# Performance work log

Hardware: AMD Instinct MI355X
Metric: run time of the kernel (lower is better)

Reference implementation:

```python
import jax, jax.numpy as jnp
import numpy as np

N_ADDR = 400000
N_TX = 400000
E = 1500000
F_IN = 64
HID = 32
OUT = 2


def _sage(x_src, x_dst, ei, Wl, bl, Wr, n_dst):
    # SAGEConv: mean-aggregate source feats over incoming edges, then
    # out = lin_l(agg) + lin_r(x_dst). Nodes with no in-edges get agg=0.
    src, dst = ei[0], ei[1]
    msg = x_src[src]                                            # [E, F]
    s = jax.ops.segment_sum(msg, dst, num_segments=n_dst)       # [N_dst, F]
    cnt = jax.ops.segment_sum(jnp.ones((ei.shape[1], 1), x_src.dtype), dst,
                              num_segments=n_dst)               # [N_dst, 1]
    agg = s / jnp.maximum(cnt, 1.0)
    return agg @ Wl + bl + x_dst @ Wr


def setup_inputs() -> dict:
    key = jax.random.key(0)
    ks = jax.random.split(key, 24)
    d = {}
    d['x_addr'] = jax.random.normal(ks[0], (N_ADDR, F_IN), jnp.float32)
    d['x_tx'] = jax.random.normal(ks[1], (N_TX, F_IN), jnp.float32)
    d['ei_at'] = jax.random.randint(ks[2], (2, E), 0, N_ADDR)   # addr->tx (src idx < N_ADDR, dst idx < N_TX)
    d['ei_ta'] = jax.random.randint(ks[3], (2, E), 0, N_TX)     # tx->addr
    def w(k, i, o):
        return jax.random.normal(k, (i, o), jnp.float32) * (1.0 / np.sqrt(i))
    d['w1_tx_l'] = w(ks[4], F_IN, HID); d['b1_tx'] = jnp.zeros((HID,), jnp.float32)
    d['w1_tx_r'] = w(ks[5], F_IN, HID)
    d['w1_ad_l'] = w(ks[6], F_IN, HID); d['b1_ad'] = jnp.zeros((HID,), jnp.float32)
    d['w1_ad_r'] = w(ks[7], F_IN, HID)
    d['w2_tx_l'] = w(ks[8], HID, HID); d['b2_tx'] = jnp.zeros((HID,), jnp.float32)
    d['w2_tx_r'] = w(ks[9], HID, HID)
    d['w2_ad_l'] = w(ks[10], HID, HID); d['b2_ad'] = jnp.zeros((HID,), jnp.float32)
    d['w2_ad_r'] = w(ks[11], HID, HID)
    d['w3_tx_l'] = w(ks[12], HID, HID); d['b3_tx'] = jnp.zeros((HID,), jnp.float32)
    d['w3_tx_r'] = w(ks[13], HID, HID)
    d['w3_ad_l'] = w(ks[14], HID, HID); d['b3_ad'] = jnp.zeros((HID,), jnp.float32)
    d['w3_ad_r'] = w(ks[15], HID, HID)
    d['w_out'] = w(ks[16], HID, OUT); d['b_out'] = jnp.zeros((OUT,), jnp.float32)
    return d


def reference(x_addr, x_tx, ei_at, ei_ta,
              w1_tx_l, b1_tx, w1_tx_r, w1_ad_l, b1_ad, w1_ad_r,
              w2_tx_l, b2_tx, w2_tx_r, w2_ad_l, b2_ad, w2_ad_r,
              w3_tx_l, b3_tx, w3_tx_r, w3_ad_l, b3_ad, w3_ad_r,
              w_out, b_out):
    # Layer 1 (both node types updated simultaneously from previous x_dict)
    tx = jax.nn.relu(_sage(x_addr, x_tx, ei_at, w1_tx_l, b1_tx, w1_tx_r, N_TX))
    ad = jax.nn.relu(_sage(x_tx, x_addr, ei_ta, w1_ad_l, b1_ad, w1_ad_r, N_ADDR))
    # Layer 2
    tx2 = jax.nn.relu(_sage(ad, tx, ei_at, w2_tx_l, b2_tx, w2_tx_r, N_TX))
    ad2 = jax.nn.relu(_sage(tx, ad, ei_ta, w2_ad_l, b2_ad, w2_ad_r, N_ADDR))
    # Layer 3
    ad3 = jax.nn.relu(_sage(tx2, ad2, ei_ta, w3_ad_l, b3_ad, w3_ad_r, N_ADDR))
    # Final classifier on 'addr' nodes (dropout is identity at inference)
    return ad3 @ w_out + b_out
```

## Files before the change

### kernel.cpp

```cpp
#include <hip/hip_runtime.h>

#define NADDR 400000
#define NTX   400000
#define NEDGE 1500000
#define FIN   64
#define HID   32
#define NB    1563
#define LSTR  36
#define HSTR  36
#define NND   400000

static inline int cdiv_host(long a, int b) { return (int)((a + b - 1) / b); }

__device__ __forceinline__ unsigned short f2bf(float f) {
    unsigned b = __float_as_uint(f);
    b += 0x7FFFu + ((b >> 16) & 1u);
    return (unsigned short)(b >> 16);
}
__device__ __forceinline__ float bf2f(unsigned short s) {
    return __uint_as_float(((unsigned)s) << 16);
}


__global__ void k_hist(const int* __restrict__ at_dst, const int* __restrict__ ta_dst,
                       int* __restrict__ bcnt , int GH) {
    __shared__ int h[NB];
    bool wh = blockIdx.x >= GH;
    int blk = blockIdx.x - (wh ? GH : 0);
    const int* dst = wh ? ta_dst : at_dst;
    for (int i = threadIdx.x; i < NB; i += 256) h[i] = 0;
    __syncthreads();
    for (long e = (long)blk * 256 + threadIdx.x; e < NEDGE; e += (long)GH * 256)
        atomicAdd(&h[dst[e] >> 8], 1);
    __syncthreads();
    int* g = bcnt + (wh ? NB : 0);
    for (int i = threadIdx.x; i < NB; i += 256) {
        int v = h[i];
        if (v) atomicAdd(&g[i], v);
    }
}

__global__ void k_scan_nb(const int* __restrict__ bcnt, int* __restrict__ bbase,
                          int* __restrict__ gcur) {
    __shared__ int sm[256];
    __shared__ int carry;
    int w = blockIdx.x;
    int t = threadIdx.x;
    if (t == 0) carry = 0;
    __syncthreads();
    for (int base = 0; base < NB; base += 256) {
        int i = base + t;
        int v = (i < NB) ? bcnt[w * NB + i] : 0;
        sm[t] = v;
        __syncthreads();
        for (int off = 1; off < 256; off <<= 1) {
            int x = (t >= off) ? sm[t - off] : 0;
            __syncthreads();
            sm[t] += x;
            __syncthreads();
        }
        int excl = sm[t] - v + carry;
        if (i < NB) { bbase[w * (NB + 1) + i] = excl; gcur[w * NB + i] = excl; }
        int tot = sm[255];
        __syncthreads();
        if (t == 0) carry += tot;
        __syncthreads();
    }
    if (t == 0) bbase[w * (NB + 1) + NB] = NEDGE;
}

__global__ void k_dist(const int* __restrict__ ei_at, const int* __restrict__ ei_ta,
                       int* __restrict__ gcur, unsigned* __restrict__ eb_at,
                       unsigned* __restrict__ eb_ta, int GD) {
    __shared__ int h[NB];
    __shared__ int bs[NB];
    bool wh = blockIdx.x >= GD;
    int blk = blockIdx.x - (wh ? GD : 0);
    const int* ei = wh ? ei_ta : ei_at;
    unsigned* eb = wh ? eb_ta : eb_at;
    for (int i = threadIdx.x; i < NB; i += 256) h[i] = 0;
    __syncthreads();
    long e0 = (long)blk * 256 + threadIdx.x;
    long stride = (long)GD * 256;
    for (long e = e0; e < NEDGE; e += stride)
        atomicAdd(&h[ei[NEDGE + e] >> 8], 1);
    __syncthreads();
    int* gc = gcur + (wh ? NB : 0);
    for (int i = threadIdx.x; i < NB; i += 256) {
        int c = h[i];
        bs[i] = c ? atomicAdd(&gc[i], c) : 0;
        h[i] = 0;
    }
    __syncthreads();
    for (long e = e0; e < NEDGE; e += stride) {
        int d = ei[NEDGE + e];
        int s = ei[e];
        int b = d >> 8;
        int r = atomicAdd(&h[b], 1);
        eb[bs[b] + r] = ((unsigned)s << 8) | (unsigned)(d & 255);
    }
}

__global__ void k_csrb(const unsigned* __restrict__ eb_at, const unsigned* __restrict__ eb_ta,
                       const int* __restrict__ bbase,
                       int* __restrict__ rp_tx, int* __restrict__ rp_ad,
                       int* __restrict__ col_at, int* __restrict__ col_ta) {
    __shared__ int deg[256];
    __shared__ int cur[256];
    __shared__ int sm[256];
    bool wh = blockIdx.x >= NB;
    int b = blockIdx.x - (wh ? NB : 0);
    const unsigned* eb = wh ? eb_ta : eb_at;
    int* rp  = wh ? rp_ad  : rp_tx;
    int* col = wh ? col_ta : col_at;
    const int* bb = bbase + (wh ? (NB + 1) : 0);
    int e0 = bb[b], e1 = bb[b + 1];
    int t = threadIdx.x;
    deg[t] = 0;
    __syncthreads();
    for (int e = e0 + t; e < e1; e += 256)
        atomicAdd(&deg[eb[e] & 255], 1);
    __syncthreads();
    int v = deg[t];
    sm[t] = v;
    __syncthreads();
    for (int off = 1; off < 256; off <<= 1) {
        int x = (t >= off) ? sm[t - off] : 0;
        __syncthreads();
        sm[t] += x;
        __syncthreads();
    }
    int excl = sm[t] - v;
    int node = b * 256 + t;
    if (node < NND) rp[node] = e0 + excl;
    cur[t] = e0 + excl;
    __syncthreads();
    for (int e = e0 + t; e < e1; e += 256) {
        unsigned p = eb[e];
        int idx = atomicAdd(&cur[p & 255], 1);
        col[idx] = (int)(p >> 8);
    }
    if (t == 0 && b == 0) rp[NND] = NEDGE;
}

__global__ __launch_bounds__(128)
void k_preS2(const float* __restrict__ x,
             const float* __restrict__ wa, unsigned short* __restrict__ outa,
             const float* __restrict__ wb, const float* __restrict__ bb,
             float* __restrict__ outb, int n) {
    __shared__ alignas(16) float xs[128 * LSTR];
    int t = threadIdx.x;
    long row0 = (long)blockIdx.x * 128;

    float aa[HID], ab[HID];
#pragma unroll
    for (int j = 0; j < HID; ++j) { aa[j] = 0.0f; ab[j] = bb[j]; }

    for (int kt = 0; kt < FIN / 32; ++kt) {
        if (kt) __syncthreads();
#pragma unroll
        for (int sub = 0; sub < 8; ++sub) {
            int f = sub * 128 + t;
            int r = f >> 3, k4 = f & 7;
            long gr = row0 + r;
            if (gr >= n) gr = n - 1;
            *(float4*)(&xs[r * LSTR + k4 * 4]) =
                *(const float4*)(x + gr * FIN + kt * 32 + k4 * 4);
        }
        __syncthreads();
        float xr[32];
#pragma unroll
        for (int q = 0; q < 8; ++q) {
            float4 v = *(const float4*)(&xs[t * LSTR + q * 4]);
            xr[q * 4] = v.x; xr[q * 4 + 1] = v.y; xr[q * 4 + 2] = v.z; xr[q * 4 + 3] = v.w;
        }
        const float* wka = wa + kt * 32 * HID;
        const float* wkb = wb + kt * 32 * HID;
#pragma unroll
        for (int k = 0; k < 32; ++k) {
            float xk = xr[k];
            const float* ra = wka + k * HID;
            const float* rb = wkb + k * HID;
#pragma unroll
            for (int j = 0; j < HID; ++j) {
                aa[j] = __builtin_fmaf(xk, ra[j], aa[j]);
                ab[j] = __builtin_fmaf(xk, rb[j], ab[j]);
            }
        }
    }

    long gr = row0 + t;
    if (gr >= n) return;
    {
        uint4* o = (uint4*)(outa + gr * HID);
#pragma unroll
        for (int q = 0; q < 4; ++q) {
            unsigned w0 = (unsigned)f2bf(aa[q * 8 + 0]) | ((unsigned)f2bf(aa[q * 8 + 1]) << 16);
            unsigned w1 = (unsigned)f2bf(aa[q * 8 + 2]) | ((unsigned)f2bf(aa[q * 8 + 3]) << 16);
            unsigned w2 = (unsigned)f2bf(aa[q * 8 + 4]) | ((unsigned)f2bf(aa[q * 8 + 5]) << 16);
            unsigned w3 = (unsigned)f2bf(aa[q * 8 + 6]) | ((unsigned)f2bf(aa[q * 8 + 7]) << 16);
            o[q] = make_uint4(w0, w1, w2, w3);
        }
    }
    {
        float* o = outb + gr * HID;
#pragma unroll
        for (int j = 0; j < HID; j += 4)
            *(float4*)(o + j) = make_float4(ab[j], ab[j + 1], ab[j + 2], ab[j + 3]);
    }
}

template<int EP, bool A16>
__global__ __launch_bounds__(256)
void k_aggE(const int* __restrict__ rp, const int* __restrict__ col,
            const unsigned short* __restrict__ preL, const float* preR,
            const float* __restrict__ wA, const float* __restrict__ bA, void* outA,
            const float* __restrict__ wB, const float* __restrict__ bB, float* outB,
            int n) {
    __shared__ alignas(16) float hh[256 * HSTR];
    int t = threadIdx.x;
    long row0 = (long)blockIdx.x * 256;
    int u = t & 7;
    int lnb = t >> 3;

    for (int bi = 0; bi < 8; ++bi) {
        int ln = bi * 32 + lnb;
        long g = row0 + ln;
        if (g < n) {
            int p0 = rp[g], p1 = rp[g + 1];
            float ax = 0.0f, ay = 0.0f, az = 0.0f, aw = 0.0f;
            for (int k = p0; k < p1; k += 8) {
                int last = p1 - 1;
                int idx[8];
#pragma unroll
                for (int q = 0; q < 8; ++q) {
                    int e = k + q;
                    idx[q] = col[e < p1 ? e : last];
                }
                ushort4 v[8];
#pragma unroll
                for (int q = 0; q < 8; ++q)
                    v[q] = *(const ushort4*)(preL + (size_t)idx[q] * HID + u * 4);
#pragma unroll
                for (int q = 0; q < 8; ++q) {
                    if (k + q < p1) {
                        ax += bf2f(v[q].x); ay += bf2f(v[q].y);
                        az += bf2f(v[q].z); aw += bf2f(v[q].w);
                    }
                }
            }
            float inv = 1.0f / fmaxf((float)(p1 - p0), 1.0f);
            float4 r = *(const float4*)(preR + (size_t)g * HID + u * 4);
            float* hp = &hh[ln * HSTR + u * 4];
            hp[0] = fmaxf(__builtin_fmaf(ax, inv, r.x), 0.0f);
            hp[1] = fmaxf(__builtin_fmaf(ay, inv, r.y), 0.0f);
            hp[2] = fmaxf(__builtin_fmaf(az, inv, r.z), 0.0f);
            hp[3] = fmaxf(__builtin_fmaf(aw, inv, r.w), 0.0f);
        }
    }
    __syncthreads();

    long gd = row0 + t;
    if (gd >= n) return;
    float rrow[32];
#pragma unroll
    for (int q = 0; q < 8; ++q) {
        float4 v = *(const float4*)(&hh[t * HSTR + q * 4]);
        rrow[q * 4] = v.x; rrow[q * 4 + 1] = v.y;
        rrow[q * 4 + 2] = v.z; rrow[q * 4 + 3] = v.w;
    }

    if (EP == 2) {
        float o0 = bA[0], o1 = bA[1];
#pragma unroll
        for (int k = 0; k < HID; ++k) {
            o0 = __builtin_fmaf(rrow[k], wA[k * 2 + 0], o0);
            o1 = __builtin_fmaf(rrow[k], wA[k * 2 + 1], o1);
        }
        float* oo = (float*)outA;
        oo[gd * 2 + 0] = o0;
        oo[gd * 2 + 1] = o1;
        return;
    }

    {
        float acc[HID];
#pragma unroll
        for (int j = 0; j < HID; ++j) acc[j] = bA ? bA[j] : 0.0f;
#pragma unroll
        for (int k = 0; k < HID; ++k) {
            float rk = rrow[k];
            const float* wr = wA + k * HID;
#pragma unroll
            for (int j = 0; j < HID; ++j) acc[j] = __builtin_fmaf(rk, wr[j], acc[j]);
        }
        if (A16) {
            uint4* o = (uint4*)((unsigned short*)outA + gd * HID);
#pragma unroll
            for (int q = 0; q < 4; ++q) {
                unsigned w0 = (unsigned)f2bf(acc[q * 8 + 0]) | ((unsigned)f2bf(acc[q * 8 + 1]) << 16);
                unsigned w1 = (unsigned)f2bf(acc[q * 8 + 2]) | ((unsigned)f2bf(acc[q * 8 + 3]) << 16);
                unsigned w2 = (unsigned)f2bf(acc[q * 8 + 4]) | ((unsigned)f2bf(acc[q * 8 + 5]) << 16);
                unsigned w3 = (unsigned)f2bf(acc[q * 8 + 6]) | ((unsigned)f2bf(acc[q * 8 + 7]) << 16);
                o[q] = make_uint4(w0, w1, w2, w3);
            }
        } else {
            float* o = (float*)outA + (size_t)gd * HID;
#pragma unroll
            for (int j = 0; j < HID; j += 4)
                *(float4*)(o + j) = make_float4(acc[j], acc[j + 1], acc[j + 2], acc[j + 3]);
        }
    }
    if (EP == 0) {
        float acc[HID];
#pragma unroll
        for (int j = 0; j < HID; ++j) acc[j] = bB[j];
#pragma unroll
        for (int k = 0; k < HID; ++k) {
            float rk = rrow[k];
            const float* wr = wB + k * HID;
#pragma unroll
            for (int j = 0; j < HID; ++j) acc[j] = __builtin_fmaf(rk, wr[j], acc[j]);
        }
        float* o = outB + (size_t)gd * HID;
#pragma unroll
        for (int j = 0; j < HID; j += 4)
            *(float4*)(o + j) = make_float4(acc[j], acc[j + 1], acc[j + 2], acc[j + 3]);
    }
}


extern "C" void kernel_launch(void* const* d_in, const int* in_sizes, int n_in,
                              void* d_out, int out_size, void* d_ws, size_t ws_size,
                              hipStream_t stream) {
    const float* x_addr  = (const float*)d_in[0];
    const float* x_tx    = (const float*)d_in[1];
    const int*   ei_at   = (const int*)d_in[2];
    const int*   ei_ta   = (const int*)d_in[3];
    const float* w1_tx_l = (const float*)d_in[4];  const float* b1_tx = (const float*)d_in[5];
    const float* w1_tx_r = (const float*)d_in[6];
    const float* w1_ad_l = (const float*)d_in[7];  const float* b1_ad = (const float*)d_in[8];
    const float* w1_ad_r = (const float*)d_in[9];
    const float* w2_tx_l = (const float*)d_in[10]; const float* b2_tx = (const float*)d_in[11];
    const float* w2_tx_r = (const float*)d_in[12];
    const float* w2_ad_l = (const float*)d_in[13]; const float* b2_ad = (const float*)d_in[14];
    const float* w2_ad_r = (const float*)d_in[15];
    const float* w3_ad_l = (const float*)d_in[19]; const float* b3_ad = (const float*)d_in[20];
    const float* w3_ad_r = (const float*)d_in[21];
    const float* w_out   = (const float*)d_in[22]; const float* b_out = (const float*)d_in[23];
    float* out = (float*)d_out;

    char* base = (char*)d_ws;
    int* bcnt   = (int*)base;  base += (size_t)(2 * NB) * 4;
    int* bbase  = (int*)base;  base += (size_t)(2 * (NB + 1)) * 4;
    int* gcur   = (int*)base;  base += (size_t)(2 * NB) * 4;
    int* rp_tx  = (int*)base;  base += (size_t)(NND + 1) * 4;
    int* rp_ad  = (int*)base;  base += (size_t)(NND + 1) * 4;
    int* col_at = (int*)base;  base += (size_t)NEDGE * 4;
    int* col_ta = (int*)base;  base += (size_t)NEDGE * 4;
    base = (char*)(((size_t)base + 255) & ~(size_t)255);
    const size_t SLOT = (size_t)NND * HID;
    char* S0 = base;
    unsigned* eb_at = (unsigned*)base;
    unsigned* eb_ta = eb_at + (size_t)NEDGE;
    char* S1 = S0 + SLOT * 4;
    char* S2 = S1 + SLOT * 4;
    char* S3 = S2 + SLOT * 4;
    char* S4 = S3 + SLOT * 4;

    unsigned short* pLtx  = (unsigned short*)S1;
    unsigned short* pLad  = (unsigned short*)S2;
    float*          pRad  = (float*)S3;
    float*          pRtx  = (float*)S4;
    unsigned short* pLad2 = (unsigned short*)S0;
    unsigned short* pLtx2 = (unsigned short*)S1;
    float*          pRad2 = (float*)S3;
    unsigned short* pLad3 = (unsigned short*)S2;
    float*          pRad3 = (float*)S3;

    dim3 blk(256);
    dim3 blk128(128);
    int gS = cdiv_host(NND, 128);
    int gB = cdiv_host(NND, 256);
    const int GH = 96, GD = 192;

    hipMemsetAsync(bcnt, 0, (size_t)(2 * NB) * 4, stream);
    k_hist<<<2 * GH, blk, 0, stream>>>(ei_at + NEDGE, ei_ta + NEDGE, bcnt, GH);
    k_scan_nb<<<2, blk, 0, stream>>>(bcnt, bbase, gcur);
    k_dist<<<2 * GD, blk, 0, stream>>>(ei_at, ei_ta, gcur, eb_at, eb_ta, GD);
    k_csrb<<<2 * NB, blk, 0, stream>>>(eb_at, eb_ta, bbase, rp_tx, rp_ad, col_at, col_ta);

    k_preS2<<<gS, blk128, 0, stream>>>(x_addr, w1_tx_l, pLtx, w1_ad_r, b1_ad, pRad, NADDR);
    k_preS2<<<gS, blk128, 0, stream>>>(x_tx,  w1_ad_l, pLad, w1_tx_r, b1_tx, pRtx, NTX);

    k_aggE<0, true><<<gB, blk, 0, stream>>>(rp_tx, col_at, pLtx, pRtx,
                                            w2_ad_l, nullptr, pLad2,
                                            w2_tx_r, b2_tx, pRtx, NTX);
    k_aggE<0, true><<<gB, blk, 0, stream>>>(rp_ad, col_ta, pLad, pRad,
                                            w2_tx_l, nullptr, pLtx2,
                                            w2_ad_r, b2_ad, pRad2, NADDR);

    k_aggE<1, true><<<gB, blk, 0, stream>>>(rp_tx, col_at, pLtx2, pRtx,
                                            w3_ad_l, nullptr, pLad3,
                                            nullptr, nullptr, nullptr, NTX);
    k_aggE<1, false><<<gB, blk, 0, stream>>>(rp_ad, col_ta, pLad2, pRad2,
                                             w3_ad_r, b3_ad, pRad3,
                                             nullptr, nullptr, nullptr, NADDR);

    k_aggE<2, false><<<gB, blk, 0, stream>>>(rp_ad, col_ta, pLad3, pRad3,
                                             w_out, b_out, out,
                                             nullptr, nullptr, nullptr, NADDR);
}
```

Measured before the change: 799.4 us.

## Rewrite layer-1 projection kernel with register-resident weights per output column

The layer-1 dense projection kernel is restructured. Before, each thread computed a full 32-wide output row from an LDS-staged input tile and read weights from global memory. Now each lane owns one output column, keeps that column's 64 weights for both matrices in registers, and walks 8 rows, broadcast-loading each input row as float4 across the 32-lane team. This removes the LDS staging, the barriers and the repeated weight loads, and gives coalesced per-column stores. The cost is 128 weight registers per thread and redundant input reads across lanes, which depend on cache broadcast.

```diff
diff --git a/kernel.cpp b/kernel.cpp
--- a/kernel.cpp
+++ b/kernel.cpp
@@ -6,7 +6,6 @@
 #define FIN   64
 #define HID   32
 #define NB    1563
-#define LSTR  36
 #define HSTR  36
 #define NND   400000
 
@@ -143,70 +142,44 @@
     if (t == 0 && b == 0) rp[NND] = NEDGE;
 }
 
-__global__ __launch_bounds__(128)
-void k_preS2(const float* __restrict__ x,
-             const float* __restrict__ wa, unsigned short* __restrict__ outa,
-             const float* __restrict__ wb, const float* __restrict__ bb,
-             float* __restrict__ outb, int n) {
-    __shared__ alignas(16) float xs[128 * LSTR];
+__global__ __launch_bounds__(256)
+void k_preW(const float* __restrict__ x,
+            const float* __restrict__ wa, unsigned short* __restrict__ outa,
+            const float* __restrict__ wb, const float* __restrict__ bb,
+            float* __restrict__ outb, int n) {
     int t = threadIdx.x;
-    long row0 = (long)blockIdx.x * 128;
-
-    float aa[HID], ab[HID];
-#pragma unroll
-    for (int j = 0; j < HID; ++j) { aa[j] = 0.0f; ab[j] = bb[j]; }
-
-    for (int kt = 0; kt < FIN / 32; ++kt) {
-        if (kt) __syncthreads();
-#pragma unroll
-        for (int sub = 0; sub < 8; ++sub) {
-            int f = sub * 128 + t;
-            int r = f >> 3, k4 = f & 7;
-            long gr = row0 + r;
-            if (gr >= n) gr = n - 1;
-            *(float4*)(&xs[r * LSTR + k4 * 4]) =
-                *(const float4*)(x + gr * FIN + kt * 32 + k4 * 4);
-        }
-        __syncthreads();
-        float xr[32];
-#pragma unroll
-        for (int q = 0; q < 8; ++q) {
-            float4 v = *(const float4*)(&xs[t * LSTR + q * 4]);
-            xr[q * 4] = v.x; xr[q * 4 + 1] = v.y; xr[q * 4 + 2] = v.z; xr[q * 4 + 3] = v.w;
-        }
-        const float* wka = wa + kt * 32 * HID;
-        const float* wkb = wb + kt * 32 * HID;
-#pragma unroll
-        for (int k = 0; k < 32; ++k) {
-            float xk = xr[k];
-            const float* ra = wka + k * HID;
-            const float* rb = wkb + k * HID;
-#pragma unroll
-            for (int j = 0; j < HID; ++j) {
-                aa[j] = __builtin_fmaf(xk, ra[j], aa[j]);
-                ab[j] = __builtin_fmaf(xk, rb[j], ab[j]);
-            }
-        }
-    }
-
-    long gr = row0 + t;
-    if (gr >= n) return;
-    {
-        uint4* o = (uint4*)(outa + gr * HID);
-#pragma unroll
-        for (int q = 0; q < 4; ++q) {
-            unsigned w0 = (unsigned)f2bf(aa[q * 8 + 0]) | ((unsigned)f2bf(aa[q * 8 + 1]) << 16);
-            unsigned w1 = (unsigned)f2bf(aa[q * 8 + 2]) | ((unsigned)f2bf(aa[q * 8 + 3]) << 16);
-            unsigned w2 = (unsigned)f2bf(aa[q * 8 + 4]) | ((unsigned)f2bf(aa[q * 8 + 5]) << 16);
-            unsigned w3 = (unsigned)f2bf(aa[q * 8 + 6]) | ((unsigned)f2bf(aa[q * 8 + 7]) << 16);
-            o[q] = make_uint4(w0, w1, w2, w3);
-        }
-    }
-    {
-        float* o = outb + gr * HID;
-#pragma unroll
-        for (int j = 0; j < HID; j += 4)
-            *(float4*)(o + j) = make_float4(ab[j], ab[j + 1], ab[j + 2], ab[j + 3]);
+    int j = t & 31;
+    int team = t >> 5;
+    long row0 = (long)blockIdx.x * 64 + (long)team * 8;
+
+    float wAr[FIN], wBr[FIN];
+#pragma unroll
+    for (int k = 0; k < FIN; ++k) {
+        wAr[k] = wa[k * HID + j];
+        wBr[k] = wb[k * HID + j];
+    }
+    float bbj = bb[j];
+
+#pragma unroll
+    for (int rr = 0; rr < 8; ++rr) {
+        long row = row0 + rr;
+        if (row >= n) break;
+        const float4* xr = (const float4*)(x + row * FIN);
+        float aa = 0.0f, ab = bbj;
+#pragma unroll
+        for (int k4 = 0; k4 < FIN / 4; ++k4) {
+            float4 v = xr[k4];
+            aa = __builtin_fmaf(v.x, wAr[4 * k4 + 0], aa);
+            ab = __builtin_fmaf(v.x, wBr[4 * k4 + 0], ab);
+            aa = __builtin_fmaf(v.y, wAr[4 * k4 + 1], aa);
+            ab = __builtin_fmaf(v.y, wBr[4 * k4 + 1], ab);
+            aa = __builtin_fmaf(v.z, wAr[4 * k4 + 2], aa);
+            ab = __builtin_fmaf(v.z, wBr[4 * k4 + 2], ab);
+            aa = __builtin_fmaf(v.w, wAr[4 * k4 + 3], aa);
+            ab = __builtin_fmaf(v.w, wBr[4 * k4 + 3], ab);
+        }
+        outa[row * HID + j] = f2bf(aa);
+        outb[row * HID + j] = ab;
     }
 }
 
@@ -379,8 +352,7 @@
     float*          pRad3 = (float*)S3;
 
     dim3 blk(256);
-    dim3 blk128(128);
-    int gS = cdiv_host(NND, 128);
+    int gW = cdiv_host(NND, 64);
     int gB = cdiv_host(NND, 256);
     const int GH = 96, GD = 192;
 
@@ -390,8 +362,8 @@
     k_dist<<<2 * GD, blk, 0, stream>>>(ei_at, ei_ta, gcur, eb_at, eb_ta, GD);
     k_csrb<<<2 * NB, blk, 0, stream>>>(eb_at, eb_ta, bbase, rp_tx, rp_ad, col_at, col_ta);
 
-    k_preS2<<<gS, blk128, 0, stream>>>(x_addr, w1_tx_l, pLtx, w1_ad_r, b1_ad, pRad, NADDR);
-    k_preS2<<<gS, blk128, 0, stream>>>(x_tx,  w1_ad_l, pLad, w1_tx_r, b1_tx, pRtx, NTX);
+    k_preW<<<gW, blk, 0, stream>>>(x_addr, w1_tx_l, pLtx, w1_ad_r, b1_ad, pRad, NADDR);
+    k_preW<<<gW, blk, 0, stream>>>(x_tx,  w1_ad_l, pLad, w1_tx_r, b1_tx, pRtx, NTX);
 
     k_aggE<0, true><<<gB, blk, 0, stream>>>(rp_tx, col_at, pLtx, pRtx,
                                             w2_ad_l, nullptr, pLad2,
```

Result: slower. 826.2 us (+3.3%).

## Coalesce preS2 stores via LDS and pair-process nodes in aggregation gather

Applied to the files above, without the earlier changes.

The pre-projection kernel now stages its bf16 and fp32 outputs through shared memory so global stores are coalesced row-contiguous, and it drops the tail clamp on input rows. The aggregation kernel processes two destination nodes per iteration with a fixed 8-edge unrolled gather plus a scalar tail loop, which puts more independent loads in flight per thread. The cost is extra shared-memory syncs and some redundant loads for low-degree nodes. Removing the row clamp assumes n is a multiple of 128, which would read and write out of bounds otherwise.

```diff
diff --git a/kernel.cpp b/kernel.cpp
--- a/kernel.cpp
+++ b/kernel.cpp
@@ -19,6 +19,9 @@
 }
 __device__ __forceinline__ float bf2f(unsigned short s) {
     return __uint_as_float(((unsigned)s) << 16);
+}
+__device__ __forceinline__ unsigned pack2bf(float a, float b) {
+    return (unsigned)f2bf(a) | ((unsigned)f2bf(b) << 16);
 }
 
 
@@ -162,10 +165,8 @@
         for (int sub = 0; sub < 8; ++sub) {
             int f = sub * 128 + t;
             int r = f >> 3, k4 = f & 7;
-            long gr = row0 + r;
-            if (gr >= n) gr = n - 1;
             *(float4*)(&xs[r * LSTR + k4 * 4]) =
-                *(const float4*)(x + gr * FIN + kt * 32 + k4 * 4);
+                *(const float4*)(x + (row0 + r) * FIN + kt * 32 + k4 * 4);
         }
         __syncthreads();
         float xr[32];
@@ -189,24 +190,28 @@
         }
     }
 
-    long gr = row0 + t;
-    if (gr >= n) return;
-    {
-        uint4* o = (uint4*)(outa + gr * HID);
-#pragma unroll
-        for (int q = 0; q < 4; ++q) {
-            unsigned w0 = (unsigned)f2bf(aa[q * 8 + 0]) | ((unsigned)f2bf(aa[q * 8 + 1]) << 16);
-            unsigned w1 = (unsigned)f2bf(aa[q * 8 + 2]) | ((unsigned)f2bf(aa[q * 8 + 3]) << 16);
-            unsigned w2 = (unsigned)f2bf(aa[q * 8 + 4]) | ((unsigned)f2bf(aa[q * 8 + 5]) << 16);
-            unsigned w3 = (unsigned)f2bf(aa[q * 8 + 6]) | ((unsigned)f2bf(aa[q * 8 + 7]) << 16);
-            o[q] = make_uint4(w0, w1, w2, w3);
-        }
-    }
-    {
-        float* o = outb + gr * HID;
-#pragma unroll
-        for (int j = 0; j < HID; j += 4)
-            *(float4*)(o + j) = make_float4(ab[j], ab[j + 1], ab[j + 2], ab[j + 3]);
+    __syncthreads();
+    unsigned* lu = (unsigned*)xs;
+#pragma unroll
+    for (int q = 0; q < 16; ++q)
+        lu[t * 17 + q] = pack2bf(aa[2 * q], aa[2 * q + 1]);
+    __syncthreads();
+    unsigned* oa32 = (unsigned*)outa + row0 * 16;
+#pragma unroll
+    for (int k = 0; k < 16; ++k) {
+        int gi = k * 128 + t;
+        oa32[gi] = lu[(gi >> 4) * 17 + (gi & 15)];
+    }
+    __syncthreads();
+#pragma unroll
+    for (int j = 0; j < HID; j += 4)
+        *(float4*)(&xs[t * LSTR + j]) = make_float4(ab[j], ab[j + 1], ab[j + 2], ab[j + 3]);
+    __syncthreads();
+#pragma unroll
+    for (int sub = 0; sub < 8; ++sub) {
+        int f = sub * 128 + t;
+        int r = f >> 3, k4 = f & 7;
+        *(float4*)(outb + (row0 + r) * HID + k4 * 4) = *(const float4*)(&xs[r * LSTR + k4 * 4]);
     }
 }
 
@@ -223,39 +228,74 @@
     int u = t & 7;
     int lnb = t >> 3;
 
-    for (int bi = 0; bi < 8; ++bi) {
-        int ln = bi * 32 + lnb;
-        long g = row0 + ln;
-        if (g < n) {
-            int p0 = rp[g], p1 = rp[g + 1];
-            float ax = 0.0f, ay = 0.0f, az = 0.0f, aw = 0.0f;
-            for (int k = p0; k < p1; k += 8) {
-                int last = p1 - 1;
-                int idx[8];
-#pragma unroll
-                for (int q = 0; q < 8; ++q) {
-                    int e = k + q;
-                    idx[q] = col[e < p1 ? e : last];
-                }
-                ushort4 v[8];
-#pragma unroll
-                for (int q = 0; q < 8; ++q)
-                    v[q] = *(const ushort4*)(preL + (size_t)idx[q] * HID + u * 4);
-#pragma unroll
-                for (int q = 0; q < 8; ++q) {
-                    if (k + q < p1) {
-                        ax += bf2f(v[q].x); ay += bf2f(v[q].y);
-                        az += bf2f(v[q].z); aw += bf2f(v[q].w);
-                    }
-                }
+#pragma unroll
+    for (int bp = 0; bp < 4; ++bp) {
+        int lnA = (2 * bp) * 32 + lnb;
+        int lnB = (2 * bp + 1) * 32 + lnb;
+        long gA = row0 + lnA;
+        long gB = row0 + lnB;
+        bool okA = gA < n, okB = gB < n;
+        long cA = okA ? gA : (n - 1);
+        long cB = okB ? gB : (n - 1);
+        int a0 = rp[cA], a1 = rp[cA + 1];
+        int b0 = rp[cB], b1 = rp[cB + 1];
+        int cntA = a1 - a0, cntB = b1 - b0;
+
+        int ia[8], ib[8];
+#pragma unroll
+        for (int q = 0; q < 8; ++q) {
+            int ea = a0 + (q < cntA ? q : (cntA > 0 ? cntA - 1 : 0));
+            int eb = b0 + (q < cntB ? q : (cntB > 0 ? cntB - 1 : 0));
+            ia[q] = col[ea < NEDGE ? ea : NEDGE - 1];
+            ib[q] = col[eb < NEDGE ? eb : NEDGE - 1];
+        }
+        ushort4 va[8], vb[8];
+#pragma unroll
+        for (int q = 0; q < 8; ++q) {
+            va[q] = *(const ushort4*)(preL + (size_t)ia[q] * HID + u * 4);
+            vb[q] = *(const ushort4*)(preL + (size_t)ib[q] * HID + u * 4);
+        }
+        float axA = 0, ayA = 0, azA = 0, awA = 0;
+        float axB = 0, ayB = 0, azB = 0, awB = 0;
+#pragma unroll
+        for (int q = 0; q < 8; ++q) {
+            if (q < cntA) {
+                axA += bf2f(va[q].x); ayA += bf2f(va[q].y);
+                azA += bf2f(va[q].z); awA += bf2f(va[q].w);
             }
-            float inv = 1.0f / fmaxf((float)(p1 - p0), 1.0f);
-            float4 r = *(const float4*)(preR + (size_t)g * HID + u * 4);
-            float* hp = &hh[ln * HSTR + u * 4];
-            hp[0] = fmaxf(__builtin_fmaf(ax, inv, r.x), 0.0f);
-            hp[1] = fmaxf(__builtin_fmaf(ay, inv, r.y), 0.0f);
-            hp[2] = fmaxf(__builtin_fmaf(az, inv, r.z), 0.0f);
-            hp[3] = fmaxf(__builtin_fmaf(aw, inv, r.w), 0.0f);
+            if (q < cntB) {
+                axB += bf2f(vb[q].x); ayB += bf2f(vb[q].y);
+                azB += bf2f(vb[q].z); awB += bf2f(vb[q].w);
+            }
+        }
+        for (int k = a0 + 8; k < a1; ++k) {
+            int s = col[k];
+            ushort4 v = *(const ushort4*)(preL + (size_t)s * HID + u * 4);
+            axA += bf2f(v.x); ayA += bf2f(v.y); azA += bf2f(v.z); awA += bf2f(v.w);
+        }
+        for (int k = b0 + 8; k < b1; ++k) {
+            int s = col[k];
+            ushort4 v = *(const ushort4*)(preL + (size_t)s * HID + u * 4);
+            axB += bf2f(v.x); ayB += bf2f(v.y); azB += bf2f(v.z); awB += bf2f(v.w);
+        }
+
+        if (okA) {
+            float inv = 1.0f / fmaxf((float)cntA, 1.0f);
+            float4 r = *(const float4*)(preR + (size_t)gA * HID + u * 4);
+            float* hp = &hh[lnA * HSTR + u * 4];
+            hp[0] = fmaxf(__builtin_fmaf(axA, inv, r.x), 0.0f);
+            hp[1] = fmaxf(__builtin_fmaf(ayA, inv, r.y), 0.0f);
+            hp[2] = fmaxf(__builtin_fmaf(azA, inv, r.z), 0.0f);
+            hp[3] = fmaxf(__builtin_fmaf(awA, inv, r.w), 0.0f);
+        }
+        if (okB) {
+            float inv = 1.0f / fmaxf((float)cntB, 1.0f);
+            float4 r = *(const float4*)(preR + (size_t)gB * HID + u * 4);
+            float* hp = &hh[lnB * HSTR + u * 4];
+            hp[0] = fmaxf(__builtin_fmaf(axB, inv, r.x), 0.0f);
+            hp[1] = fmaxf(__builtin_fmaf(ayB, inv, r.y), 0.0f);
+            hp[2] = fmaxf(__builtin_fmaf(azB, inv, r.z), 0.0f);
+            hp[3] = fmaxf(__builtin_fmaf(awB, inv, r.w), 0.0f);
         }
     }
     __syncthreads();
@@ -298,10 +338,10 @@
             uint4* o = (uint4*)((unsigned short*)outA + gd * HID);
 #pragma unroll
             for (int q = 0; q < 4; ++q) {
-                unsigned w0 = (unsigned)f2bf(acc[q * 8 + 0]) | ((unsigned)f2bf(acc[q * 8 + 1]) << 16);
-                unsigned w1 = (unsigned)f2bf(acc[q * 8 + 2]) | ((unsigned)f2bf(acc[q * 8 + 3]) << 16);
-                unsigned w2 = (unsigned)f2bf(acc[q * 8 + 4]) | ((unsigned)f2bf(acc[q * 8 + 5]) << 16);
-                unsigned w3 = (unsigned)f2bf(acc[q * 8 + 6]) | ((unsigned)f2bf(acc[q * 8 + 7]) << 16);
+                unsigned w0 = pack2bf(acc[q * 8 + 0], acc[q * 8 + 1]);
+                unsigned w1 = pack2bf(acc[q * 8 + 2], acc[q * 8 + 3]);
+                unsigned w2 = pack2bf(acc[q * 8 + 4], acc[q * 8 + 5]);
+                unsigned w3 = pack2bf(acc[q * 8 + 6], acc[q * 8 + 7]);
                 o[q] = make_uint4(w0, w1, w2, w3);
             }
         } else {
```

Result: slower. 892.0 us (+11.6%).
